# Kernel optimization log

Hardware: AMD Instinct MI355X
Metric: run time of the kernel (lower is better)

## Reference

```python
import math
import jax, jax.numpy as jnp
import numpy as np


def setup_inputs() -> dict:
    key = jax.random.key(0)
    ks = jax.random.split(key, 5)
    B, N, D, O = 16, 16384, 256, 256
    x = jax.random.normal(ks[0], (B, N, D), dtype=jnp.float32)
    Wq = jax.random.normal(ks[1], (O, D), dtype=jnp.float32) * (1.0 / math.sqrt(D))
    bq = jax.random.normal(ks[2], (O,), dtype=jnp.float32) * 0.01
    Wk = jax.random.normal(ks[3], (O, D), dtype=jnp.float32) * (1.0 / math.sqrt(D))
    bk = jax.random.normal(ks[4], (O,), dtype=jnp.float32) * 0.01
    return {"x": x, "Wq": Wq, "bq": bq, "Wk": Wk, "bk": bk}


def reference(x, Wq, bq, Wk, bk):
    # x: [B, N, D]; Wq/Wk: [O, D] (torch nn.Linear layout), bq/bk: [O]
    O = Wq.shape[0]
    scale = 1.0 / math.sqrt(O)
    q = jnp.einsum('bnd,od->bno', x, Wq) + bq          # [B, N, O]
    k = jnp.einsum('bnd,od->bno', x, Wk) + bk          # [B, N, O]
    # sum_j (q_i . k_j) == q_i . (sum_j k_j): avoid the O(N^2) score matrix
    ksum = k.sum(axis=1)                               # [B, O]
    summed_scores = jnp.einsum('bno,bo->bn', q, ksum) * scale  # [B, N]
    customer_weights = jax.nn.softmax(summed_scores, axis=-1)  # [B, N]
    aggregated_feature = jnp.einsum('bn,bnd->bd', customer_weights, x)  # [B, D]
    average_customer_weights = customer_weights.mean(axis=0)            # [N]
    return aggregated_feature, average_customer_weights
```

## Files before the change

kernel.cpp:

```cpp
#include <hip/hip_runtime.h>
#include <math.h>

#define BB 16
#define NN 16384
#define DD 256
#define NS1 128
#define NS3 128

__global__ __launch_bounds__(256) void k1_xsum_part(const float* __restrict__ x,
                                                    float* __restrict__ part) {
  const int b = blockIdx.y, blk = blockIdx.x;
  const int wave = threadIdx.x >> 6, lane = threadIdx.x & 63;
  const int rows = NN / NS1;
  const float* xp = x + ((size_t)b * NN + (size_t)blk * rows) * DD;
  float4 acc = make_float4(0.f, 0.f, 0.f, 0.f);
  for (int r = wave; r < rows; r += 4) {
    float4 v = *(const float4*)(xp + (size_t)r * DD + lane * 4);
    acc.x += v.x; acc.y += v.y; acc.z += v.z; acc.w += v.w;
  }
  __shared__ float sP[4][DD];
  *(float4*)&sP[wave][lane * 4] = acc;
  __syncthreads();
  const int t = threadIdx.x;
  part[((size_t)b * NS1 + blk) * DD + t] = sP[0][t] + sP[1][t] + sP[2][t] + sP[3][t];
}

__global__ __launch_bounds__(256) void k2_prep(const float* __restrict__ part,
                                               const float* __restrict__ Wq,
                                               const float* __restrict__ bq,
                                               const float* __restrict__ Wk,
                                               const float* __restrict__ bk,
                                               float* __restrict__ v,
                                               float* __restrict__ c) {
  const int b = blockIdx.x, t = threadIdx.x;
  __shared__ float xs[DD];
  __shared__ float ks[DD];
  __shared__ float red[256];

  float acc = 0.f;
  for (int blk = 0; blk < NS1; ++blk) acc += part[((size_t)b * NS1 + blk) * DD + t];
  xs[t] = acc;
  __syncthreads();

  float kacc = (float)NN * bk[t];
  const float* wkrow = Wk + (size_t)t * DD;
  for (int j = 0; j < DD; ++j) kacc += wkrow[j] * xs[j];
  ks[t] = kacc;
  __syncthreads();

  float vacc = 0.f;
  for (int o = 0; o < DD; ++o) vacc += Wq[(size_t)o * DD + t] * ks[o];
  v[b * DD + t] = vacc;

  red[t] = bq[t] * ks[t];
  __syncthreads();
  for (int s = 128; s > 0; s >>= 1) {
    if (t < s) red[t] += red[t + s];
    __syncthreads();
  }
  if (t == 0) c[b] = red[0];
}

__global__ __launch_bounds__(256) void k3_main(const float* __restrict__ x,
                                               const float* __restrict__ v,
                                               const float* __restrict__ c,
                                               float* __restrict__ scores,
                                               float* __restrict__ pm,
                                               float* __restrict__ pz,
                                               float* __restrict__ pP) {
  const int b = blockIdx.y, blk = blockIdx.x;
  const int wave = threadIdx.x >> 6, lane = threadIdx.x & 63;
  const float scale = 0.0625f;

  const float4 vl = *(const float4*)(v + b * DD + lane * 4);
  const float cb = c[b];
  const int rows_per_block = NN / NS3;
  const int rows_per_wave = rows_per_block / 4;
  const int n0 = blk * rows_per_block + wave * rows_per_wave;
  const float* xb = x + (size_t)b * NN * DD;

  float m = -INFINITY, Z = 0.f;
  float4 P = make_float4(0.f, 0.f, 0.f, 0.f);

  for (int i = 0; i < rows_per_wave; ++i) {
    const int n = n0 + i;
    float4 xr = *(const float4*)(xb + (size_t)n * DD + lane * 4);
    float dot = xr.x * vl.x + xr.y * vl.y + xr.z * vl.z + xr.w * vl.w;
#pragma unroll
    for (int off = 32; off >= 1; off >>= 1) dot += __shfl_xor(dot, off, 64);
    const float s = (dot + cb) * scale;
    if (lane == 0) scores[(size_t)b * NN + n] = s;

    const float mn = fmaxf(m, s);
    const float alpha = __expf(m - mn);
    const float e = __expf(s - mn);
    Z = Z * alpha + e;
    P.x = P.x * alpha + e * xr.x;
    P.y = P.y * alpha + e * xr.y;
    P.z = P.z * alpha + e * xr.z;
    P.w = P.w * alpha + e * xr.w;
    m = mn;
  }

  __shared__ float sm[4], sz[4];
  __shared__ float sP[4][DD];
  *(float4*)&sP[wave][lane * 4] = P;
  if (lane == 0) { sm[wave] = m; sz[wave] = Z; }
  __syncthreads();

  const int t = threadIdx.x;
  const float M = fmaxf(fmaxf(sm[0], sm[1]), fmaxf(sm[2], sm[3]));
  const float e0 = __expf(sm[0] - M), e1 = __expf(sm[1] - M);
  const float e2 = __expf(sm[2] - M), e3 = __expf(sm[3] - M);
  const float Pd = sP[0][t] * e0 + sP[1][t] * e1 + sP[2][t] * e2 + sP[3][t] * e3;
  const size_t idx = (size_t)b * NS3 + blk;
  pP[idx * DD + t] = Pd;
  if (t == 0) {
    pm[idx] = M;
    pz[idx] = sz[0] * e0 + sz[1] * e1 + sz[2] * e2 + sz[3] * e3;
  }
}

__global__ __launch_bounds__(256) void k4_final(const float* __restrict__ pm,
                                                const float* __restrict__ pz,
                                                const float* __restrict__ pP,
                                                float* __restrict__ out_agg,
                                                float* __restrict__ Mb,
                                                float* __restrict__ rZb) {
  const int b = blockIdx.x, t = threadIdx.x;
  __shared__ float red[256];
  const size_t base = (size_t)b * NS3;

  red[t] = (t < NS3) ? pm[base + t] : -INFINITY;
  __syncthreads();
  for (int s = 128; s > 0; s >>= 1) {
    if (t < s) red[t] = fmaxf(red[t], red[t + s]);
    __syncthreads();
  }
  const float M = red[0];
  __syncthreads();

  red[t] = (t < NS3) ? pz[base + t] * __expf(pm[base + t] - M) : 0.f;
  __syncthreads();
  for (int s = 128; s > 0; s >>= 1) {
    if (t < s) red[t] += red[t + s];
    __syncthreads();
  }
  const float Z = red[0];
  const float rZ = 1.f / Z;

  float acc = 0.f;
  for (int blk = 0; blk < NS3; ++blk)
    acc += pP[(base + blk) * DD + t] * __expf(pm[base + blk] - M);
  out_agg[b * DD + t] = acc * rZ;
  if (t == 0) { Mb[b] = M; rZb[b] = rZ; }
}

__global__ __launch_bounds__(256) void k5_avgw(const float* __restrict__ scores,
                                               const float* __restrict__ Mb,
                                               const float* __restrict__ rZb,
                                               float* __restrict__ out_w) {
  const int n = blockIdx.x * blockDim.x + threadIdx.x;
  __shared__ float sM[BB], sR[BB];
  if (threadIdx.x < BB) { sM[threadIdx.x] = Mb[threadIdx.x]; sR[threadIdx.x] = rZb[threadIdx.x]; }
  __syncthreads();
  float acc = 0.f;
#pragma unroll
  for (int b = 0; b < BB; ++b)
    acc += __expf(scores[(size_t)b * NN + n] - sM[b]) * sR[b];
  out_w[n] = acc * (1.f / BB);
}

extern "C" void kernel_launch(void* const* d_in, const int* in_sizes, int n_in,
                              void* d_out, int out_size, void* d_ws, size_t ws_size,
                              hipStream_t stream) {
  const float* x  = (const float*)d_in[0];
  const float* Wq = (const float*)d_in[1];
  const float* bq = (const float*)d_in[2];
  const float* Wk = (const float*)d_in[3];
  const float* bk = (const float*)d_in[4];

  float* out  = (float*)d_out;
  float* agg  = out;
  float* avgw = out + BB * DD;

  float* ws = (float*)d_ws;
  float* part   = ws;  ws += (size_t)BB * NS1 * DD;
  float* v      = ws;  ws += BB * DD;
  float* c      = ws;  ws += BB;
  float* scores = ws;  ws += (size_t)BB * NN;
  float* pm     = ws;  ws += BB * NS3;
  float* pz     = ws;  ws += BB * NS3;
  float* pP     = ws;  ws += (size_t)BB * NS3 * DD;
  float* Mb     = ws;  ws += BB;
  float* rZb    = ws;  ws += BB;

  k1_xsum_part<<<dim3(NS1, BB), 256, 0, stream>>>(x, part);
  k2_prep<<<BB, 256, 0, stream>>>(part, Wq, bq, Wk, bk, v, c);
  k3_main<<<dim3(NS3, BB), 256, 0, stream>>>(x, v, c, scores, pm, pz, pP);
  k4_final<<<BB, 256, 0, stream>>>(pm, pz, pP, agg, Mb, rZb);
  k5_avgw<<<NN / 256, 256, 0, stream>>>(scores, Mb, rZb, avgw);
}
```

Before: 122.1 us.

## Merge final softmax kernels, vectorize Wk matvec, reverse k3 block order for cache reuse

Combines the final aggregation and average-weight kernels into one launch; the weight blocks recompute each batch's max and normalizer from the per-block partials with wave shuffles, so there is no longer a dependency on a separate kernel. This removes one launch and its serialization at the cost of redundant small reductions in every weight block. The Wk row dot product in the prep kernel now uses float4 loads with unrolling. The main kernel walks blocks in reverse order so the tail of x, touched last by the first pass, may still be cache-resident when the second pass begins.

```diff
diff --git a/kernel.cpp b/kernel.cpp
--- a/kernel.cpp
+++ b/kernel.cpp
@@ -43,8 +43,12 @@
   __syncthreads();
 
   float kacc = (float)NN * bk[t];
-  const float* wkrow = Wk + (size_t)t * DD;
-  for (int j = 0; j < DD; ++j) kacc += wkrow[j] * xs[j];
+  const float4* wkrow4 = (const float4*)(Wk + (size_t)t * DD);
+#pragma unroll 4
+  for (int j4 = 0; j4 < DD / 4; ++j4) {
+    const float4 w = wkrow4[j4];
+    kacc += w.x * xs[4 * j4] + w.y * xs[4 * j4 + 1] + w.z * xs[4 * j4 + 2] + w.w * xs[4 * j4 + 3];
+  }
   ks[t] = kacc;
   __syncthreads();
 
@@ -68,7 +72,8 @@
                                                float* __restrict__ pm,
                                                float* __restrict__ pz,
                                                float* __restrict__ pP) {
-  const int b = blockIdx.y, blk = blockIdx.x;
+  const int b = BB - 1 - blockIdx.y;
+  const int blk = NS3 - 1 - blockIdx.x;
   const int wave = threadIdx.x >> 6, lane = threadIdx.x & 63;
   const float scale = 0.0625f;
 
@@ -121,54 +126,69 @@
   }
 }
 
-__global__ __launch_bounds__(256) void k4_final(const float* __restrict__ pm,
-                                                const float* __restrict__ pz,
-                                                const float* __restrict__ pP,
-                                                float* __restrict__ out_agg,
-                                                float* __restrict__ Mb,
-                                                float* __restrict__ rZb) {
-  const int b = blockIdx.x, t = threadIdx.x;
-  __shared__ float red[256];
-  const size_t base = (size_t)b * NS3;
-
-  red[t] = (t < NS3) ? pm[base + t] : -INFINITY;
-  __syncthreads();
-  for (int s = 128; s > 0; s >>= 1) {
-    if (t < s) red[t] = fmaxf(red[t], red[t + s]);
-    __syncthreads();
-  }
-  const float M = red[0];
-  __syncthreads();
-
-  red[t] = (t < NS3) ? pz[base + t] * __expf(pm[base + t] - M) : 0.f;
-  __syncthreads();
-  for (int s = 128; s > 0; s >>= 1) {
-    if (t < s) red[t] += red[t + s];
-    __syncthreads();
-  }
-  const float Z = red[0];
-  const float rZ = 1.f / Z;
-
-  float acc = 0.f;
-  for (int blk = 0; blk < NS3; ++blk)
-    acc += pP[(base + blk) * DD + t] * __expf(pm[base + blk] - M);
-  out_agg[b * DD + t] = acc * rZ;
-  if (t == 0) { Mb[b] = M; rZb[b] = rZ; }
-}
-
-__global__ __launch_bounds__(256) void k5_avgw(const float* __restrict__ scores,
-                                               const float* __restrict__ Mb,
-                                               const float* __restrict__ rZb,
-                                               float* __restrict__ out_w) {
-  const int n = blockIdx.x * blockDim.x + threadIdx.x;
-  __shared__ float sM[BB], sR[BB];
-  if (threadIdx.x < BB) { sM[threadIdx.x] = Mb[threadIdx.x]; sR[threadIdx.x] = rZb[threadIdx.x]; }
-  __syncthreads();
-  float acc = 0.f;
-#pragma unroll
-  for (int b = 0; b < BB; ++b)
-    acc += __expf(scores[(size_t)b * NN + n] - sM[b]) * sR[b];
-  out_w[n] = acc * (1.f / BB);
+__global__ __launch_bounds__(256) void k45_final(const float* __restrict__ pm,
+                                                 const float* __restrict__ pz,
+                                                 const float* __restrict__ pP,
+                                                 const float* __restrict__ scores,
+                                                 float* __restrict__ out_agg,
+                                                 float* __restrict__ out_w) {
+  const int t = threadIdx.x;
+  if (blockIdx.x < BB) {
+    const int b = blockIdx.x;
+    __shared__ float red[256];
+    const size_t base = (size_t)b * NS3;
+
+    red[t] = (t < NS3) ? pm[base + t] : -INFINITY;
+    __syncthreads();
+    for (int s = 128; s > 0; s >>= 1) {
+      if (t < s) red[t] = fmaxf(red[t], red[t + s]);
+      __syncthreads();
+    }
+    const float M = red[0];
+    __syncthreads();
+
+    red[t] = (t < NS3) ? pz[base + t] * __expf(pm[base + t] - M) : 0.f;
+    __syncthreads();
+    for (int s = 128; s > 0; s >>= 1) {
+      if (t < s) red[t] += red[t + s];
+      __syncthreads();
+    }
+    const float rZ = 1.f / red[0];
+
+    float acc = 0.f;
+    for (int blk = 0; blk < NS3; ++blk)
+      acc += pP[(base + blk) * DD + t] * __expf(pm[base + blk] - M);
+    out_agg[b * DD + t] = acc * rZ;
+  } else {
+    const int wb = blockIdx.x - BB;
+    __shared__ float sM[BB], sR[BB];
+    const int b = t >> 4;
+    const int i = t & 15;
+    const size_t base = (size_t)b * NS3 + i * 8;
+
+    float mloc = -INFINITY;
+#pragma unroll
+    for (int k = 0; k < 8; ++k) mloc = fmaxf(mloc, pm[base + k]);
+#pragma unroll
+    for (int off = 8; off >= 1; off >>= 1) mloc = fmaxf(mloc, __shfl_xor(mloc, off, 64));
+    const float M = mloc;
+
+    float zloc = 0.f;
+#pragma unroll
+    for (int k = 0; k < 8; ++k) zloc += pz[base + k] * __expf(pm[base + k] - M);
+#pragma unroll
+    for (int off = 8; off >= 1; off >>= 1) zloc += __shfl_xor(zloc, off, 64);
+
+    if (i == 0) { sM[b] = M; sR[b] = 1.f / zloc; }
+    __syncthreads();
+
+    const int n = wb * 256 + t;
+    float acc = 0.f;
+#pragma unroll
+    for (int bb = 0; bb < BB; ++bb)
+      acc += __expf(scores[(size_t)bb * NN + n] - sM[bb]) * sR[bb];
+    out_w[n] = acc * (1.f / BB);
+  }
 }
 
 extern "C" void kernel_launch(void* const* d_in, const int* in_sizes, int n_in,
@@ -192,12 +212,9 @@
   float* pm     = ws;  ws += BB * NS3;
   float* pz     = ws;  ws += BB * NS3;
   float* pP     = ws;  ws += (size_t)BB * NS3 * DD;
-  float* Mb     = ws;  ws += BB;
-  float* rZb    = ws;  ws += BB;
 
   k1_xsum_part<<<dim3(NS1, BB), 256, 0, stream>>>(x, part);
   k2_prep<<<BB, 256, 0, stream>>>(part, Wq, bq, Wk, bk, v, c);
   k3_main<<<dim3(NS3, BB), 256, 0, stream>>>(x, v, c, scores, pm, pz, pP);
-  k4_final<<<BB, 256, 0, stream>>>(pm, pz, pP, agg, Mb, rZb);
-  k5_avgw<<<NN / 256, 256, 0, stream>>>(scores, Mb, rZb, avgw);
-}
+  k45_final<<<BB + NN / 256, 256, 0, stream>>>(pm, pz, pP, scores, agg, avgw);
+}
```

Measured after the change: 119.5 us. 2.1% less time.
